# Optimization experiments

Measured on AMD Instinct MI355X. Metric: run time of the kernel, lower is better.

Reference implementation:

```python
import jax, jax.numpy as jnp
import numpy as np

B, L, F, H = 2048, 256, 64, 128  # trees, leaves per tree, features, hidden


def _xavier(k, shape, gain=np.sqrt(2.0)):
    fan_in, fan_out = shape
    bound = gain * np.sqrt(6.0 / (fan_in + fan_out))
    return jax.random.uniform(k, shape, jnp.float32, -bound, bound)


def setup_inputs() -> dict:
    key = jax.random.key(0)
    ks = jax.random.split(key, 6)
    return {
        "x": jax.random.normal(ks[0], (B, L, F), jnp.float32),
        "W_leaf": _xavier(ks[1], (F, H)),
        "b_leaf": jnp.zeros((H,), jnp.float32),
        "W_nl": _xavier(ks[2], (3 * H, H)),
        "b_nl": jnp.zeros((H,), jnp.float32),
        "W1": _xavier(ks[3], (H, H)),
        "b1": jnp.zeros((H,), jnp.float32),
        "W2": _xavier(ks[4], (H, H)),
        "b2": jnp.zeros((H,), jnp.float32),
        "W3": _xavier(ks[5], (H, 1)),
        "b3": jnp.zeros((1,), jnp.float32),
    }


def reference(x, W_leaf, b_leaf, W_nl, b_nl, W1, b1, W2, b2, W3, b3):
    # Depth-batched encoding of complete binary trees.
    leaf = lambda d: jax.nn.relu(d @ W_leaf + b_leaf)
    data = x                     # [B, n, F] node data at current level
    h = leaf(data)               # [B, n, H] leaf encodings
    while h.shape[1] > 1:        # fixed log2(L) structural levels
        data = data[:, 0::2] + data[:, 1::2]          # internal node data = sum of children
        u = leaf(data)                                # u = leaf(left.data + right.data)
        hlr_u = jnp.concatenate([h[:, 0::2], h[:, 1::2], u], axis=-1)  # [B, n/2, 3H]
        h = jax.nn.relu(hlr_u @ W_nl + b_nl)          # nonleaf(h_l, h_r, u)
    enc = h[:, 0]                # [B, H] root encoding
    z = jax.nn.relu(enc @ W1 + b1)
    z = jax.nn.relu(z @ W2 + b2)
    return (z @ W3 + b3).squeeze(-1)  # [B] per-tree logit
```

## Files before the change

kernel.cpp:

```cpp
#include <hip/hip_runtime.h>
#include <hip/hip_bf16.h>
#include <stdint.h>


#define B_TOT 2048
#define LL    256
#define FF    64
#define HH    128
#define LF    (LL*FF)
#define BC    8
#define NTHR  512
#define NSUB  16

typedef __bf16 v8bf __attribute__((ext_vector_type(8)));
typedef float  v4f  __attribute__((ext_vector_type(4)));

#define XB_OFF    0
#define XB2_OFF   16384
#define DB_OFF    32768
#define DB2_OFF   49152
#define HA_OFF    61440
#define HB_OFF    94208
#define U_OFF     110592
#define HCUR_OFF  126976
#define DCUR_OFF  131072
#define HSTK_OFF  133120
#define DSTK_OFF  149504
#define BIAS_OFF  157696
#define LDS_BYTES 159744

__device__ __forceinline__ uint32_t swz256(uint32_t row, uint32_t b){
    return (row*256u + b) ^ ((row & 7u) << 4);
}
__device__ __forceinline__ uint32_t swz128(uint32_t row, uint32_t b){
    return (row*128u + b) ^ ((row & 7u) << 4);
}
__device__ __forceinline__ v4f mfma16(v8bf a, v8bf b, v4f c){
    return __builtin_amdgcn_mfma_f32_16x16x32_bf16(a, b, c, 0, 0, 0);
}
__device__ __forceinline__ uint32_t pk2(float a, float b){
    uint32_t lo = (uint32_t)__builtin_bit_cast(unsigned short, (__bf16)a);
    uint32_t hi = (uint32_t)__builtin_bit_cast(unsigned short, (__bf16)b);
    return lo | (hi << 16);
}
__device__ __forceinline__ uint2 pk4(v4f v){
    return make_uint2(pk2(v[0], v[1]), pk2(v[2], v[3]));
}

__device__ __forceinline__ v8bf ldW(const float* __restrict__ W, int k0, int n0){
    uint32_t lane = threadIdx.x & 63u;
    int n = n0 + (int)(lane & 15u);
    int k = k0 + (int)((lane >> 4) << 3);
    v8bf r;
    #pragma unroll
    for (int j = 0; j < 8; ++j) r[j] = (__bf16)W[(k + j)*HH + n];
    return r;
}

__device__ __forceinline__ v8bf ldX(const char* xb, uint32_t row0, uint32_t mt,
                                    uint32_t kf, uint32_t realrows){
    uint32_t lane = threadIdx.x & 63u;
    uint32_t rl = mt*16u + (lane & 15u);
    if (rl >= realrows){
        v8bf z;
        #pragma unroll
        for (int j = 0; j < 8; ++j) z[j] = (__bf16)0.0f;
        return z;
    }
    return *reinterpret_cast<const v8bf*>(xb + swz128(row0 + rl, kf*64u + ((lane>>4)<<4)));
}

__device__ __forceinline__ v8bf ldH(const char* buf, uint32_t kf){
    uint32_t lane = threadIdx.x & 63u;
    return *reinterpret_cast<const v8bf*>(buf + swz256(lane & 15u,
                                          kf*64u + ((lane>>4)<<4)));
}

__device__ __forceinline__ v8bf ldA_nl(const char* hprev, const char* ub,
                                       uint32_t mt, uint32_t kf){
    uint32_t lane = threadIdx.x & 63u, r = lane & 15u;
    uint32_t kb = (kf & 3u)*64u + ((lane >> 4) << 4);
    uint32_t sec = kf >> 2;
    if (sec < 2u){
        uint32_t row = mt*32u + ((r >> 3) << 4) + sec*8u + (r & 7u);
        return *reinterpret_cast<const v8bf*>(hprev + swz256(row, kb));
    }
    return *reinterpret_cast<const v8bf*>(ub + swz256(mt*16u + r, kb));
}

__device__ __forceinline__ void epi(char* dst, uint32_t row0, v4f acc, int nt,
                                    const float* bias){
    uint32_t lane = threadIdx.x & 63u;
    uint32_t col = (uint32_t)nt*16u + (lane & 15u);
    float bv = bias[col];
    uint32_t r0 = row0 + ((lane >> 4) << 2);
    #pragma unroll
    for (int r = 0; r < 4; ++r){
        float v = fmaxf(acc[r] + bv, 0.f);
        *reinterpret_cast<__bf16*>(dst + swz256(r0 + r, col*2u)) = (__bf16)v;
    }
}

template<int MTN>
__device__ __forceinline__ void gemm_x(const char* xb, uint32_t row0, uint32_t realrows,
                                       char* dst, uint32_t mtB, const v8bf (&wlf)[2],
                                       int nt, const float* bias){
    v4f acc[MTN];
    #pragma unroll
    for (int i = 0; i < MTN; ++i) acc[i] = (v4f){0,0,0,0};
    #pragma unroll
    for (uint32_t kf = 0; kf < 2; ++kf){
        v8bf a[MTN];
        #pragma unroll
        for (int i = 0; i < MTN; ++i) a[i] = ldX(xb, row0, mtB + i, kf, realrows);
        #pragma unroll
        for (int i = 0; i < MTN; ++i) acc[i] = mfma16(a[i], wlf[kf], acc[i]);
    }
    #pragma unroll
    for (int i = 0; i < MTN; ++i) epi(dst, (mtB + i)*16u, acc[i], nt, bias);
}

template<int MTN>
__device__ __forceinline__ void gemm_nl(const char* hprev, const char* ub, char* dst,
                                        uint32_t mtB, const v8bf (&wnl)[12],
                                        int nt, const float* bias){
    v4f acc[MTN];
    #pragma unroll
    for (int i = 0; i < MTN; ++i) acc[i] = (v4f){0,0,0,0};
    #pragma unroll
    for (uint32_t kf = 0; kf < 12; ++kf){
        v8bf a[MTN];
        #pragma unroll
        for (int i = 0; i < MTN; ++i) a[i] = ldA_nl(hprev, ub, mtB + i, kf);
        #pragma unroll
        for (int i = 0; i < MTN; ++i) acc[i] = mfma16(a[i], wnl[kf], acc[i]);
    }
    #pragma unroll
    for (int i = 0; i < MTN; ++i) epi(dst, (mtB + i)*16u, acc[i], nt, bias);
}

__global__ __launch_bounds__(NTHR)
__attribute__((amdgpu_waves_per_eu(2, 2)))
void recnn_kernel(const float* __restrict__ Xg,
                  const float* __restrict__ Wleaf, const float* __restrict__ bleaf,
                  const float* __restrict__ Wnl,   const float* __restrict__ bnl,
                  const float* __restrict__ W1g,   const float* __restrict__ b1g,
                  const float* __restrict__ W2g,   const float* __restrict__ b2g,
                  const float* __restrict__ W3g,   const float* __restrict__ b3g,
                  float* __restrict__ Yg)
{
    __shared__ __align__(16) char lds[LDS_BYTES];
    const int t    = threadIdx.x;
    const int wave = t >> 6;
    const int base = blockIdx.x * BC;

    char*  XB   = lds + XB_OFF;
    char*  XB2  = lds + XB2_OFF;
    char*  DB   = lds + DB_OFF;
    char*  DB2  = lds + DB2_OFF;
    char*  HA   = lds + HA_OFF;
    char*  HB   = lds + HB_OFF;
    char*  Ub   = lds + U_OFF;
    char*  HCUR = lds + HCUR_OFF;
    char*  DCUR = lds + DCUR_OFF;
    char*  HSTK = lds + HSTK_OFF;
    char*  DSTK = lds + DSTK_OFF;
    float* BL   = (float*)(lds + BIAS_OFF);
    float* BN   = BL + 128;
    float* B1L  = BL + 256;
    float* B2L  = BL + 384;

    if (t < 128){
        BL[t]  = bleaf[t];
        BN[t]  = bnl[t];
        B1L[t] = b1g[t];
        B2L[t] = b2g[t];
    }

    const int nt = wave;
    const int n0 = wave << 4;
    v8bf wlf[2], wnl[12];
    #pragma unroll
    for (int kf = 0; kf < 2; ++kf)  wlf[kf] = ldW(Wleaf, kf*32, n0);
    #pragma unroll
    for (int kf = 0; kf < 12; ++kf) wnl[kf] = ldW(Wnl, kf*32, n0);

    auto sum_level = [&](char* dstF, uint32_t dRow0, uint32_t xRow0,
                         const char* srcF, uint32_t sRow0, int outrows){
        int total = outrows * 16;
        for (int idx = t; idx < total; idx += NTHR){
            uint32_t row = (uint32_t)(idx >> 4), q = (uint32_t)(idx & 15);
            uint32_t n = row >> 3, b = row & 7u;
            v4f a = *reinterpret_cast<const v4f*>(srcF + swz256(sRow0 + n*16u + b,      q*16u));
            v4f c = *reinterpret_cast<const v4f*>(srcF + swz256(sRow0 + n*16u + 8u + b, q*16u));
            v4f sv = a + c;
            *reinterpret_cast<v4f*>(dstF + swz256(dRow0 + row, q*16u)) = sv;
            *reinterpret_cast<uint2*>(XB2 + swz128(xRow0 + row, q*8u)) = pk4(sv);
        }
    };

    int sp = 0;
    for (int s = 0; s < NSUB; ++s){
        if (s > 0){
            ((uint2*)(HSTK + sp*4096))[t]    = ((const uint2*)HCUR)[t];
            ((uint32_t*)(DSTK + sp*2048))[t] = ((const uint32_t*)DCUR)[t];
            ++sp;
        }
        #pragma unroll
        for (int k = 0; k < 2; ++k){
            int idx = t + k*NTHR;
            uint32_t rp = (uint32_t)(idx >> 4), q = (uint32_t)(idx & 15);
            uint32_t n = rp >> 3, b = rp & 7u;
            const float* gp = Xg + (size_t)(base + b)*LF + (size_t)(s*16 + 2*n)*FF + q*4;
            v4f xA = *reinterpret_cast<const v4f*>(gp);
            v4f xC = *reinterpret_cast<const v4f*>(gp + FF);
            uint32_t rowA = n*16u + b;
            *reinterpret_cast<uint2*>(XB + swz128(rowA,      q*8u)) = pk4(xA);
            *reinterpret_cast<uint2*>(XB + swz128(rowA + 8u, q*8u)) = pk4(xC);
            v4f sv = xA + xC;
            *reinterpret_cast<v4f*>(DB + swz256(rp, q*16u)) = sv;
            *reinterpret_cast<uint2*>(XB2 + swz128(rp, q*8u)) = pk4(sv);
        }
        __syncthreads();

        gemm_x<4>(XB, 0, 128, HA, 0, wlf, nt, BL);
        gemm_x<4>(XB, 0, 128, HA, 4, wlf, nt, BL);
        sum_level(DB2, 0, 64, DB, 0, 32);
        __syncthreads();
        gemm_x<4>(XB2, 0, 64, Ub, 0, wlf, nt, BL);
        sum_level(DB, 0, 96, DB2, 0, 16);
        __syncthreads();
        gemm_nl<4>(HA, Ub, HB, 0, wnl, nt, BN);
        sum_level(DB2, 32, 112, DB, 0, 8);
        __syncthreads();
        gemm_x<2>(XB2, 64, 32, Ub, 0, wlf, nt, BL);
        __syncthreads();
        gemm_nl<2>(HB, Ub, HA, 0, wnl, nt, BN);
        __syncthreads();
        gemm_x<1>(XB2, 96, 16, Ub, 0, wlf, nt, BL);
        __syncthreads();
        gemm_nl<1>(HA, Ub, HB, 0, wnl, nt, BN);
        __syncthreads();
        gemm_x<1>(XB2, 112, 8, Ub, 0, wlf, nt, BL);
        __syncthreads();
        gemm_nl<1>(HB, Ub, HCUR, 0, wnl, nt, BN);
        {
            uint32_t row = (uint32_t)(t >> 6), f = (uint32_t)(t & 63);
            *reinterpret_cast<float*>(DCUR + swz256(row, f*4u)) =
                *reinterpret_cast<const float*>(DB2 + swz256(32u + row, f*4u));
        }
        __syncthreads();

        int nm = __builtin_ctz(s + 1);
        for (int m = 0; m < nm; ++m){
            --sp;
            const char* hl = HSTK + sp*4096;
            {
                uint32_t row = (uint32_t)(t >> 6), f = (uint32_t)(t & 63);
                float v = *reinterpret_cast<const float*>(DCUR + swz256(row, f*4u))
                        + *reinterpret_cast<const float*>(DSTK + sp*2048 + swz256(row, f*4u));
                *reinterpret_cast<float*>(DCUR + swz256(row, f*4u)) = v;
                *reinterpret_cast<__bf16*>(XB2 + swz128(120u + row, f*2u)) = (__bf16)v;
            }
            __syncthreads();
            gemm_x<1>(XB2, 120, 8, Ub, 0, wlf, nt, BL);
            __syncthreads();
            v4f c = (v4f){0,0,0,0};
            #pragma unroll
            for (uint32_t kf = 0; kf < 12; ++kf){
                const char* src = (kf < 4) ? hl : ((kf < 8) ? (const char*)HCUR
                                                            : (const char*)Ub);
                c = mfma16(ldH(src, kf & 3u), wnl[kf], c);
            }
            __syncthreads();
            epi(HCUR, 0, c, nt, BN);
            __syncthreads();
        }
    }

    {
        v8bf w1f[4], w2f[4];
        #pragma unroll
        for (int kf = 0; kf < 4; ++kf){
            w1f[kf] = ldW(W1g, kf*32, n0);
            w2f[kf] = ldW(W2g, kf*32, n0);
        }
        {
            v4f c = (v4f){0,0,0,0};
            #pragma unroll
            for (uint32_t kf = 0; kf < 4; ++kf) c = mfma16(ldH(HCUR, kf), w1f[kf], c);
            epi(Ub, 0, c, nt, B1L);
        }
        __syncthreads();
        {
            v4f c = (v4f){0,0,0,0};
            #pragma unroll
            for (uint32_t kf = 0; kf < 4; ++kf) c = mfma16(ldH(Ub, kf), w2f[kf], c);
            epi(HB, 0, c, nt, B2L);
        }
        __syncthreads();
        if (t < 64){
            float w3a = W3g[t], w3b = W3g[t + 64], b3v = b3g[0];
            #pragma unroll
            for (int r = 0; r < 8; ++r){
                float za = (float)*reinterpret_cast<const __bf16*>(HB + swz256((uint32_t)r, (uint32_t)t*2u));
                float zb = (float)*reinterpret_cast<const __bf16*>(HB + swz256((uint32_t)r, (uint32_t)(t + 64)*2u));
                float v = za*w3a + zb*w3b;
                #pragma unroll
                for (int off = 32; off >= 1; off >>= 1) v += __shfl_xor(v, off, 64);
                if (t == 0) Yg[base + r] = v + b3v;
            }
        }
    }
}

extern "C" void kernel_launch(void* const* d_in, const int* in_sizes, int n_in,
                              void* d_out, int out_size, void* d_ws, size_t ws_size,
                              hipStream_t stream){
    const float* x     = (const float*)d_in[0];
    const float* Wleaf = (const float*)d_in[1];
    const float* bleaf = (const float*)d_in[2];
    const float* Wnl   = (const float*)d_in[3];
    const float* bnl   = (const float*)d_in[4];
    const float* W1    = (const float*)d_in[5];
    const float* b1    = (const float*)d_in[6];
    const float* W2    = (const float*)d_in[7];
    const float* b2    = (const float*)d_in[8];
    const float* W3    = (const float*)d_in[9];
    const float* b3    = (const float*)d_in[10];
    float* out = (float*)d_out;

    recnn_kernel<<<B_TOT/BC, NTHR, 0, stream>>>(x, Wleaf, bleaf, Wnl, bnl,
                                                W1, b1, W2, b2, W3, b3, out);
}
```

Baseline: 129.4 us.

## Merge tree-level stages, double-buffer root state, and pack epilogue stores

The per-subtree level schedule now co-issues independent leaf GEMMs with the preceding nonleaf GEMMs into separate U buffers (U2, offset Ub). This removes several block-wide barriers per subtree. The merge loop ping-pongs the current hidden state between two buffers, so the per-iteration barriers around the epilogue are dropped except on the last step. The epilogue exchanges neighbouring lanes with shuffles so each lane writes packed 32-bit bf16 pairs instead of four scalar 16-bit stores, and the H stack shrinks to 2 KB entries, lowering LDS use. The risk is races, since the buffers reused across merge iterations now depend on fewer syncs.

```diff
diff --git a/kernel.cpp b/kernel.cpp
--- a/kernel.cpp
+++ b/kernel.cpp
@@ -19,15 +19,16 @@
 #define XB2_OFF   16384
 #define DB_OFF    32768
 #define DB2_OFF   49152
-#define HA_OFF    61440
-#define HB_OFF    94208
-#define U_OFF     110592
-#define HCUR_OFF  126976
-#define DCUR_OFF  131072
-#define HSTK_OFF  133120
-#define DSTK_OFF  149504
-#define BIAS_OFF  157696
-#define LDS_BYTES 159744
+#define HA_OFF    59392
+#define HB_OFF    92160
+#define U_OFF     108544
+#define HCA_OFF   124928
+#define HCB_OFF   129024
+#define DCUR_OFF  133120
+#define HSTK_OFF  135168
+#define DSTK_OFF  143360
+#define BIAS_OFF  151552
+#define LDS_BYTES 153600
 
 __device__ __forceinline__ uint32_t swz256(uint32_t row, uint32_t b){
     return (row*256u + b) ^ ((row & 7u) << 4);
@@ -93,12 +94,22 @@
     uint32_t lane = threadIdx.x & 63u;
     uint32_t col = (uint32_t)nt*16u + (lane & 15u);
     float bv = bias[col];
+    float v0 = fmaxf(acc[0] + bv, 0.f);
+    float v1 = fmaxf(acc[1] + bv, 0.f);
+    float v2 = fmaxf(acc[2] + bv, 0.f);
+    float v3 = fmaxf(acc[3] + bv, 0.f);
+    float p0 = __shfl_xor(v0, 1);
+    float p1 = __shfl_xor(v1, 1);
+    float p2 = __shfl_xor(v2, 1);
+    float p3 = __shfl_xor(v3, 1);
     uint32_t r0 = row0 + ((lane >> 4) << 2);
-    #pragma unroll
-    for (int r = 0; r < 4; ++r){
-        float v = fmaxf(acc[r] + bv, 0.f);
-        *reinterpret_cast<__bf16*>(dst + swz256(r0 + r, col*2u)) = (__bf16)v;
-    }
+    bool odd = (lane & 1u);
+    uint32_t w0 = odd ? pk2(p2, v2) : pk2(v0, p0);
+    uint32_t w1 = odd ? pk2(p3, v3) : pk2(v1, p1);
+    uint32_t r  = odd ? (r0 + 2u) : r0;
+    uint32_t cb = (col & ~1u) * 2u;
+    *reinterpret_cast<uint32_t*>(dst + swz256(r,      cb)) = w0;
+    *reinterpret_cast<uint32_t*>(dst + swz256(r + 1u, cb)) = w1;
 }
 
 template<int MTN>
@@ -158,10 +169,10 @@
     char*  XB2  = lds + XB2_OFF;
     char*  DB   = lds + DB_OFF;
     char*  DB2  = lds + DB2_OFF;
+    char*  U2   = lds + DB2_OFF;
     char*  HA   = lds + HA_OFF;
     char*  HB   = lds + HB_OFF;
     char*  Ub   = lds + U_OFF;
-    char*  HCUR = lds + HCUR_OFF;
     char*  DCUR = lds + DCUR_OFF;
     char*  HSTK = lds + HSTK_OFF;
     char*  DSTK = lds + DSTK_OFF;
@@ -169,6 +180,9 @@
     float* BN   = BL + 128;
     float* B1L  = BL + 256;
     float* B2L  = BL + 384;
+
+    char* hc_cur = lds + HCA_OFF;
+    char* hc_alt = lds + HCB_OFF;
 
     if (t < 128){
         BL[t]  = bleaf[t];
@@ -202,7 +216,7 @@
     int sp = 0;
     for (int s = 0; s < NSUB; ++s){
         if (s > 0){
-            ((uint2*)(HSTK + sp*4096))[t]    = ((const uint2*)HCUR)[t];
+            ((uint32_t*)(HSTK + sp*2048))[t] = ((const uint32_t*)hc_cur)[t];
             ((uint32_t*)(DSTK + sp*2048))[t] = ((const uint32_t*)DCUR)[t];
             ++sp;
         }
@@ -227,23 +241,25 @@
         gemm_x<4>(XB, 0, 128, HA, 4, wlf, nt, BL);
         sum_level(DB2, 0, 64, DB, 0, 32);
         __syncthreads();
+
         gemm_x<4>(XB2, 0, 64, Ub, 0, wlf, nt, BL);
         sum_level(DB, 0, 96, DB2, 0, 16);
         __syncthreads();
+
         gemm_nl<4>(HA, Ub, HB, 0, wnl, nt, BN);
+        gemm_x<2>(XB2, 64, 32, U2, 0, wlf, nt, BL);
         sum_level(DB2, 32, 112, DB, 0, 8);
         __syncthreads();
-        gemm_x<2>(XB2, 64, 32, Ub, 0, wlf, nt, BL);
-        __syncthreads();
-        gemm_nl<2>(HB, Ub, HA, 0, wnl, nt, BN);
-        __syncthreads();
+
+        gemm_nl<2>(HB, U2, HA, 0, wnl, nt, BN);
         gemm_x<1>(XB2, 96, 16, Ub, 0, wlf, nt, BL);
         __syncthreads();
+
         gemm_nl<1>(HA, Ub, HB, 0, wnl, nt, BN);
-        __syncthreads();
-        gemm_x<1>(XB2, 112, 8, Ub, 0, wlf, nt, BL);
-        __syncthreads();
-        gemm_nl<1>(HB, Ub, HCUR, 0, wnl, nt, BN);
+        gemm_x<1>(XB2, 112, 8, Ub + 16*256, 0, wlf, nt, BL);
+        __syncthreads();
+
+        gemm_nl<1>(HB, Ub + 16*256, hc_cur, 0, wnl, nt, BN);
         {
             uint32_t row = (uint32_t)(t >> 6), f = (uint32_t)(t & 63);
             *reinterpret_cast<float*>(DCUR + swz256(row, f*4u)) =
@@ -254,7 +270,7 @@
         int nm = __builtin_ctz(s + 1);
         for (int m = 0; m < nm; ++m){
             --sp;
-            const char* hl = HSTK + sp*4096;
+            const char* hl = HSTK + sp*2048;
             {
                 uint32_t row = (uint32_t)(t >> 6), f = (uint32_t)(t & 63);
                 float v = *reinterpret_cast<const float*>(DCUR + swz256(row, f*4u))
@@ -268,13 +284,13 @@
             v4f c = (v4f){0,0,0,0};
             #pragma unroll
             for (uint32_t kf = 0; kf < 12; ++kf){
-                const char* src = (kf < 4) ? hl : ((kf < 8) ? (const char*)HCUR
+                const char* src = (kf < 4) ? hl : ((kf < 8) ? (const char*)hc_cur
                                                             : (const char*)Ub);
                 c = mfma16(ldH(src, kf & 3u), wnl[kf], c);
             }
-            __syncthreads();
-            epi(HCUR, 0, c, nt, BN);
-            __syncthreads();
+            epi(hc_alt, 0, c, nt, BN);
+            { char* tmp = hc_cur; hc_cur = hc_alt; hc_alt = tmp; }
+            if (m == nm - 1) __syncthreads();
         }
     }
 
@@ -288,7 +304,7 @@
         {
             v4f c = (v4f){0,0,0,0};
             #pragma unroll
-            for (uint32_t kf = 0; kf < 4; ++kf) c = mfma16(ldH(HCUR, kf), w1f[kf], c);
+            for (uint32_t kf = 0; kf < 4; ++kf) c = mfma16(ldH(hc_cur, kf), w1f[kf], c);
             epi(Ub, 0, c, nt, B1L);
         }
         __syncthreads();
```

Result: slower. 147.9 us (+14.3%).
